# Kernel tuning notes

Hardware: AMD Instinct MI355X
Metric: run time of the kernel (lower is better)

## Reference

```python
import jax, jax.numpy as jnp
import numpy as np

N_NODES = 100000
N_EDGES = 1600000
IN_DIM = 256
HID = 128
N_LAYERS = 4
OUT_DIM = 7
LAMDA = 0.5
LN_EPS = 1e-5


def setup_inputs() -> dict:
    key = jax.random.key(0)
    ks = jax.random.split(key, 12)
    x = jax.random.normal(ks[0], (N_NODES, IN_DIM), jnp.float32)
    edge_index = jax.random.randint(ks[1], (2, N_EDGES), 0, N_NODES, dtype=jnp.int32)

    def unif(k, shape, fan_out):
        s = 1.0 / np.sqrt(fan_out)
        return jax.random.uniform(k, shape, jnp.float32, -s, s)

    W_proj = unif(ks[2], (IN_DIM, HID), HID)
    b_proj = unif(ks[3], (HID,), HID)
    gamma = jnp.ones((HID,), jnp.float32)
    beta = jnp.zeros((HID,), jnp.float32)
    q_w = unif(ks[4], (HID, 1), 1)
    q_b = unif(ks[5], (1,), 1)
    conv_w = unif(ks[6], (N_LAYERS, HID, HID), HID)
    cls_w = unif(ks[7], (HID, OUT_DIM), OUT_DIM)
    cls_b = unif(ks[8], (OUT_DIM,), OUT_DIM)
    return {"x": x, "edge_index": edge_index, "W_proj": W_proj, "b_proj": b_proj,
            "gamma": gamma, "beta": beta, "q_w": q_w, "q_b": q_b,
            "conv_w": conv_w, "cls_w": cls_w, "cls_b": cls_b}


def reference(x, edge_index, W_proj, b_proj, gamma, beta, q_w, q_b, conv_w, cls_w, cls_b):
    n = x.shape[0]
    row, col = edge_index[0], edge_index[1]

    # symmetric normalization: D^-1/2 A D^-1/2 with unit edge data (duplicates sum)
    deg = jax.ops.segment_sum(jnp.ones(row.shape[0], x.dtype), row, num_segments=n)
    deg = jnp.where(deg == 0, jnp.ones_like(deg), deg)  # (row_sum==0)*1 + row_sum
    d_inv_sqrt = deg ** -0.5
    ew = d_inv_sqrt[row] * d_inv_sqrt[col]  # [E]

    def spmm(h):  # out[r] += ew * h[c]
        return jax.ops.segment_sum(ew[:, None] * h[col], row, num_segments=n)

    def layernorm(h):
        mu = jnp.mean(h, axis=-1, keepdims=True)
        var = jnp.mean((h - mu) ** 2, axis=-1, keepdims=True)
        return gamma * (h - mu) * jax.lax.rsqrt(var + LN_EPS) + beta

    h0 = layernorm(x @ W_proj + b_proj)  # project + layernorm
    h = h0
    for i in range(conv_w.shape[0]):
        # dropout is identity in eval mode
        s = jax.nn.sigmoid(h @ q_w + q_b - 1.0)  # [N,1] learned gate
        theta = LAMDA / (i + 1)
        hi = spmm(h)
        support = (1.0 - s) * hi + s * h0  # AOR blend (variant=False -> r == support)
        out = theta * (support @ conv_w[i]) + (1.0 - theta) * support  # DLR
        h = layernorm(jax.nn.relu(out))
    return h @ cls_w + cls_b
```

## Files before the change

### kernel.cpp

```cpp
#include <hip/hip_runtime.h>
#include <hip/hip_bf16.h>
#include <hip/hip_fp16.h>
#include <stdint.h>

#define N_NODES 100000
#define N_EDGES 1600000
#define IN_DIM 256
#define HID 128
#define N_LAYERS 4
#define OUT_DIM 7
#define LN_EPS 1e-5f

#define BSHIFT 6
#define BROWS 64
#define NBK 1563
#define CHUNK 16384
#define NCH ((N_EDGES + CHUNK - 1) / CHUNK)

typedef __attribute__((ext_vector_type(8))) short bf16x8;
typedef __attribute__((ext_vector_type(4))) float f32x4;

__device__ inline float bf2f1(uint16_t u) {
    union { uint32_t i; float f; } a; a.i = ((uint32_t)u) << 16; return a.f;
}
__device__ inline uint16_t f2bf(float f) {
    union { float f; uint32_t i; } a; a.f = f;
    uint32_t lsb = (a.i >> 16) & 1u;
    a.i += 0x7fffu + lsb;
    return (uint16_t)(a.i >> 16);
}
__device__ inline uint32_t packq(float a, float b, float qinv) {
    int qa = __float2int_rn(a * qinv);
    int qb = __float2int_rn(b * qinv);
    return ((uint32_t)(uint16_t)(short)qa) | (((uint32_t)(uint16_t)(short)qb) << 16);
}

__device__ __host__ inline int wpack_idx(int k, int c) {
    int ksg = k >> 5, lg = (k >> 3) & 3, e = k & 7;
    int ct = c >> 4, li = c & 15;
    return ((ksg * 8 + ct) * 64 + (lg * 16 + li)) * 8 + e;
}

__global__ void k_detect(const uint32_t* __restrict__ W, int* __restrict__ flag) {
    if (threadIdx.x == 0 && blockIdx.x == 0) {
        int cnt = 0;
        for (int i = 0; i < 64; i++) {
            uint32_t lo = W[i] & 0xffffu;
            uint32_t ex = (lo >> 7) & 0xff;
            if (ex >= 0x60 && ex < 0x7c) cnt++;
        }
        *flag = (cnt < 32) ? 1 : 0;
    }
}
__global__ void k_setflag(int* __restrict__ flag, int v) {
    if (threadIdx.x == 0) *flag = v;
}

__global__ __launch_bounds__(256) void k_cvt(const void* a0, const void* a1, const void* a2,
                                             const void* a3, const void* a4, const void* a5,
                                             const void* a6, const void* a7, const void* a8,
                                             float* __restrict__ dst, const int* __restrict__ flag) {
    int t = blockIdx.x * 256 + threadIdx.x;
    if (t >= 99720) return;
    const void* src; int i; int off;
    if      (t < 32768) { src = a0; i = t;         off = 0;     }
    else if (t < 32896) { src = a1; i = t - 32768; off = 32768; }
    else if (t < 33024) { src = a2; i = t - 32896; off = 32896; }
    else if (t < 33152) { src = a3; i = t - 33024; off = 33024; }
    else if (t < 33280) { src = a4; i = t - 33152; off = 33152; }
    else if (t < 33281) { src = a5; i = t - 33280; off = 33280; }
    else if (t < 98817) { src = a6; i = t - 33281; off = 33296; }
    else if (t < 99713) { src = a7; i = t - 98817; off = 98832; }
    else                { src = a8; i = t - 99713; off = 99728; }
    float v;
    if (*flag) v = ((const float*)src)[i];
    else       v = bf2f1(((const uint16_t*)src)[i]);
    dst[off + i] = v;
}

__global__ __launch_bounds__(256) void k_wsplit(const float* __restrict__ stg,
                                                uint16_t* __restrict__ wpkhi, uint16_t* __restrict__ wpklo,
                                                uint16_t* __restrict__ cwkhi, uint16_t* __restrict__ cwklo) {
    int t = blockIdx.x * 256 + threadIdx.x;
    if (t >= 32768 + 65536) return;
    float v; size_t dst; uint16_t *ha, *la;
    if (t < 32768) {
        int k = t >> 7, c = t & 127;
        v = stg[t];
        dst = (size_t)wpack_idx(k, c); ha = wpkhi; la = wpklo;
    } else {
        int u = t - 32768;
        int L = u >> 14, rem = u & 16383;
        int k = rem >> 7, c = rem & 127;
        v = stg[33296 + u];
        dst = (size_t)L * 16384 + wpack_idx(k, c); ha = cwkhi; la = cwklo;
    }
    uint16_t hb = f2bf(v);
    uint16_t lb = f2bf(v - bf2f1(hb));
    ha[dst] = hb; la[dst] = lb;
}


__global__ __launch_bounds__(256) void k_hist(const int* __restrict__ row, int* __restrict__ hist) {
    __shared__ int lh[NBK];
    int b = blockIdx.x, tid = threadIdx.x;
    for (int i = tid; i < NBK; i += 256) lh[i] = 0;
    __syncthreads();
    int e0 = b * CHUNK;
    int lim = N_EDGES - e0; if (lim > CHUNK) lim = CHUNK;
    for (int i = tid; i < lim; i += 256) atomicAdd(&lh[row[e0 + i] >> BSHIFT], 1);
    __syncthreads();
    for (int i = tid; i < NBK; i += 256) hist[(size_t)b * NBK + i] = lh[i];
}

__global__ __launch_bounds__(128) void k_hscan(int* __restrict__ hist, int* __restrict__ totB) {
    __shared__ int s[128];
    int bkt = blockIdx.x, t = threadIdx.x;
    int v = (t < NCH) ? hist[(size_t)t * NBK + bkt] : 0;
    s[t] = v;
    __syncthreads();
    for (int off = 1; off < 128; off <<= 1) {
        int add = (t >= off) ? s[t - off] : 0;
        __syncthreads();
        s[t] += add;
        __syncthreads();
    }
    if (t < NCH) hist[(size_t)t * NBK + bkt] = s[t] - v;
    if (t == 127) totB[bkt] = s[127];
}

__global__ __launch_bounds__(256) void k_bscan(const int* __restrict__ totB,
                                               int* __restrict__ boffB, int* __restrict__ rp) {
    __shared__ int ps[256];
    int t = threadIdx.x;
    const int STRIP = 7;
    int base = t * STRIP;
    int loc[STRIP]; int sum = 0;
#pragma unroll
    for (int j = 0; j < STRIP; j++) {
        int idx = base + j;
        int v = (idx < NBK) ? totB[idx] : 0;
        loc[j] = sum; sum += v;
    }
    ps[t] = sum;
    __syncthreads();
    int v = ps[t];
    for (int off = 1; off < 256; off <<= 1) {
        int add = (t >= off) ? ps[t - off] : 0;
        __syncthreads();
        ps[t] += add;
        __syncthreads();
    }
    int excl = ps[t] - v;
#pragma unroll
    for (int j = 0; j < STRIP; j++) {
        int idx = base + j;
        if (idx < NBK) boffB[idx] = excl + loc[j];
    }
    if (t == 0) { boffB[NBK] = N_EDGES; rp[N_NODES] = N_EDGES; }
}

__global__ __launch_bounds__(256) void k_sortscat(const int* __restrict__ row, const int* __restrict__ col,
                                                  const int* __restrict__ hist, const int* __restrict__ boffB,
                                                  uint32_t* __restrict__ ebp) {
    __shared__ int dbase[NBK];
    __shared__ int lcnt[NBK];
    int b = blockIdx.x, tid = threadIdx.x;
    for (int i = tid; i < NBK; i += 256) {
        dbase[i] = boffB[i] + hist[(size_t)b * NBK + i];
        lcnt[i] = 0;
    }
    __syncthreads();
    int e0 = b * CHUNK;
    int lim = N_EDGES - e0; if (lim > CHUNK) lim = CHUNK;
    for (int i = tid; i < lim; i += 256) {
        int r = row[e0 + i], c = col[e0 + i];
        int bk = r >> BSHIFT;
        int rank = atomicAdd(&lcnt[bk], 1);
        ebp[dbase[bk] + rank] = ((uint32_t)(r & (BROWS - 1)) << 17) | (uint32_t)c;
    }
}

__global__ __launch_bounds__(256) void k_bfin(const uint32_t* __restrict__ ebp, const int* __restrict__ boffB,
                                              int* __restrict__ rp, float* __restrict__ dis,
                                              int* __restrict__ edc) {
    __shared__ int ldeg[BROWS];
    __shared__ int lcur[BROWS];
    int b = blockIdx.x, tid = threadIdx.x;
    int base = boffB[b];
    int n = boffB[b + 1] - base;
    if (tid < BROWS) ldeg[tid] = 0;
    __syncthreads();
    for (int i = tid; i < n; i += 256) atomicAdd(&ldeg[ebp[base + i] >> 17], 1);
    __syncthreads();
    if (tid == 0) {
        int run = 0;
        for (int r = 0; r < BROWS; r++) { int d = ldeg[r]; lcur[r] = run; run += d; }
    }
    __syncthreads();
    int row0 = b << BSHIFT;
    if (tid < BROWS && row0 + tid < N_NODES) {
        int d = ldeg[tid];
        rp[row0 + tid]  = base + lcur[tid];
        dis[row0 + tid] = rsqrtf((float)(d > 0 ? d : 1));
    }
    __syncthreads();
    for (int i = tid; i < n; i += 256) {
        uint32_t pk = ebp[base + i];
        int r = pk >> 17;
        int pos = atomicAdd(&lcur[r], 1);
        edc[base + pos] = (int)(pk & 0x1FFFFu);
    }
}


__global__ __launch_bounds__(256) void k_spmm(const uint32_t* __restrict__ Hq,
                                              const float* __restrict__ ScD,
                                              const float* __restrict__ H0,
                                              const int* __restrict__ rp,
                                              const int* __restrict__ edc,
                                              const float* __restrict__ S,
                                              const float* __restrict__ dis,
                                              uint16_t* __restrict__ SupHi,
                                              uint16_t* __restrict__ SupLo) {
    int wid  = (blockIdx.x * 256 + threadIdx.x) >> 6;
    int lane = threadIdx.x & 63;
    if (wid >= N_NODES) return;

    float s  = S[wid];
    float dr = dis[wid];
    float h0x = H0[(size_t)wid * 128 + lane];
    float h0y = H0[(size_t)wid * 128 + 64 + lane];

    int p0 = rp[wid], p1 = rp[wid + 1];
    float ax = 0.f, ay = 0.f;
    int p = p0;
    for (; p + 8 <= p1; p += 8) {
        int c[8]; uint32_t u[8]; float w[8];
#pragma unroll
        for (int j = 0; j < 8; j++) c[j] = edc[p + j];
#pragma unroll
        for (int j = 0; j < 8; j++) u[j] = Hq[(size_t)c[j] * 64 + lane];
#pragma unroll
        for (int j = 0; j < 8; j++) w[j] = ScD[c[j]];
#pragma unroll
        for (int j = 0; j < 8; j++) {
            ax += w[j] * (float)((int)(u[j] << 16) >> 16);
            ay += w[j] * (float)((int)u[j] >> 16);
        }
    }
    for (; p + 4 <= p1; p += 4) {
        int c[4]; uint32_t u[4]; float w[4];
#pragma unroll
        for (int j = 0; j < 4; j++) c[j] = edc[p + j];
#pragma unroll
        for (int j = 0; j < 4; j++) u[j] = Hq[(size_t)c[j] * 64 + lane];
#pragma unroll
        for (int j = 0; j < 4; j++) w[j] = ScD[c[j]];
#pragma unroll
        for (int j = 0; j < 4; j++) {
            ax += w[j] * (float)((int)(u[j] << 16) >> 16);
            ay += w[j] * (float)((int)u[j] >> 16);
        }
    }
    for (; p < p1; p++) {
        int c = edc[p];
        uint32_t u = Hq[(size_t)c * 64 + lane];
        float w = ScD[c];
        ax += w * (float)((int)(u << 16) >> 16);
        ay += w * (float)((int)u >> 16);
    }
    float f = (1.f - s) * dr;
    float ox = f * ax + s * h0x;
    float oy = f * ay + s * h0y;
    uint16_t hx = f2bf(ox), hy = f2bf(oy);
    uint16_t lx = f2bf(ox - bf2f1(hx)), ly = f2bf(oy - bf2f1(hy));
    SupHi[(size_t)wid * 128 + lane]      = hx;
    SupHi[(size_t)wid * 128 + 64 + lane] = hy;
    SupLo[(size_t)wid * 128 + lane]      = lx;
    SupLo[(size_t)wid * 128 + 64 + lane] = ly;
}


template <int KD, int MODE, int WH, int WQ, int WF>
__global__ __launch_bounds__(256, 2) void k_gemm(
    const void* __restrict__ Ax,
    const uint16_t* __restrict__ Ahi, const uint16_t* __restrict__ Alo,
    const uint16_t* __restrict__ Wh, const uint16_t* __restrict__ Wl,
    const float* __restrict__ bias, const float* __restrict__ gamma,
    const float* __restrict__ beta, const float* __restrict__ qw,
    const float* __restrict__ qb, float theta, const int* __restrict__ flag,
    const float* __restrict__ dis,
    float* __restrict__ Hout, uint32_t* __restrict__ Hq,
    float* __restrict__ Sc, float* __restrict__ S)
{
    if (*flag != WF) return;
    constexpr int F32A = (MODE == 0) ? WF : 1;
    constexpr int NKB = KD / 128;

    __shared__ __align__(16) uint16_t sWh[16384];
    __shared__ __align__(16) uint16_t sWl[16384];

    const int tid  = threadIdx.x;
    const int lane = tid & 63;
    const int wv   = tid >> 6;
    const int li   = lane & 15;
    const int lg   = lane >> 4;
    const size_t row0 = (size_t)blockIdx.x * 128;
    const int wb = wv * 32;
    size_t ar0 = row0 + wb + li;      if (ar0 >= N_NODES) ar0 = N_NODES - 1;
    size_t ar1 = row0 + wb + 16 + li; if (ar1 >= N_NODES) ar1 = N_NODES - 1;

    f32x4 acc0[8], acc1[8];
#pragma unroll
    for (int ct = 0; ct < 8; ct++) {
        acc0[ct] = (f32x4){0.f, 0.f, 0.f, 0.f};
        acc1[ct] = (f32x4){0.f, 0.f, 0.f, 0.f};
    }

    for (int kb = 0; kb < NKB; kb++) {
        if (kb) __syncthreads();
        const uint16_t* gh = Wh + kb * 16384;
#pragma unroll
        for (int it = 0; it < 8; it++) {
            int t = tid + it * 256;
            *(uint4*)(sWh + t * 8) = *(const uint4*)(gh + t * 8);
        }
        if constexpr (WF) {
            const uint16_t* gl = Wl + kb * 16384;
#pragma unroll
            for (int it = 0; it < 8; it++) {
                int t = tid + it * 256;
                *(uint4*)(sWl + t * 8) = *(const uint4*)(gl + t * 8);
            }
        }
        bf16x8 a0h[4], a1h[4], a0l[4], a1l[4];
#pragma unroll
        for (int s = 0; s < 4; s++) {
            const int koff = kb * 128 + s * 32 + lg * 8;
            if constexpr (MODE == 1) {
                a0h[s] = *(const bf16x8*)(Ahi + ar0 * KD + koff);
                a0l[s] = *(const bf16x8*)(Alo + ar0 * KD + koff);
                a1h[s] = *(const bf16x8*)(Ahi + ar1 * KD + koff);
                a1l[s] = *(const bf16x8*)(Alo + ar1 * KD + koff);
            } else if constexpr (WF) {
                const float* p0 = (const float*)Ax + ar0 * KD + koff;
                const float* p1 = (const float*)Ax + ar1 * KD + koff;
                float4 u0 = *(const float4*)p0, u1 = *(const float4*)(p0 + 4);
                float4 v0 = *(const float4*)p1, v1 = *(const float4*)(p1 + 4);
                float f0[8] = {u0.x, u0.y, u0.z, u0.w, u1.x, u1.y, u1.z, u1.w};
                float f1[8] = {v0.x, v0.y, v0.z, v0.w, v1.x, v1.y, v1.z, v1.w};
#pragma unroll
                for (int j = 0; j < 8; j++) {
                    uint16_t hb0 = f2bf(f0[j]);
                    a0h[s][j] = (short)hb0;
                    a0l[s][j] = (short)f2bf(f0[j] - bf2f1(hb0));
                    uint16_t hb1 = f2bf(f1[j]);
                    a1h[s][j] = (short)hb1;
                    a1l[s][j] = (short)f2bf(f1[j] - bf2f1(hb1));
                }
            } else {
                a0h[s] = *(const bf16x8*)((const uint16_t*)Ax + ar0 * KD + koff);
                a1h[s] = *(const bf16x8*)((const uint16_t*)Ax + ar1 * KD + koff);
            }
        }
        __syncthreads();
#pragma unroll
        for (int s = 0; s < 4; s++) {
#pragma unroll
            for (int ct = 0; ct < 8; ct++) {
                const int wo = ((s * 8 + ct) * 64 + lane) * 8;
                bf16x8 bh = *(const bf16x8*)(sWh + wo);
                acc0[ct] = __builtin_amdgcn_mfma_f32_16x16x32_bf16(a0h[s], bh, acc0[ct], 0, 0, 0);
                acc1[ct] = __builtin_amdgcn_mfma_f32_16x16x32_bf16(a1h[s], bh, acc1[ct], 0, 0, 0);
                if constexpr (F32A) {
                    acc0[ct] = __builtin_amdgcn_mfma_f32_16x16x32_bf16(a0l[s], bh, acc0[ct], 0, 0, 0);
                    acc1[ct] = __builtin_amdgcn_mfma_f32_16x16x32_bf16(a1l[s], bh, acc1[ct], 0, 0, 0);
                }
                if constexpr (WF) {
                    bf16x8 bl = *(const bf16x8*)(sWl + wo);
                    acc0[ct] = __builtin_amdgcn_mfma_f32_16x16x32_bf16(a0h[s], bl, acc0[ct], 0, 0, 0);
                    acc1[ct] = __builtin_amdgcn_mfma_f32_16x16x32_bf16(a1h[s], bl, acc1[ct], 0, 0, 0);
                }
            }
        }
    }

    float gm[8], bt_[8], qv[8], bi[8];
#pragma unroll
    for (int ct = 0; ct < 8; ct++) {
        int c = ct * 16 + li;
        gm[ct] = gamma[c]; bt_[ct] = beta[c]; qv[ct] = qw[c];
        bi[ct] = (MODE == 0) ? bias[c] : 0.f;
    }
    const float qbv = qb[0];
    const float om  = 1.f - theta;

    auto epi = [&](f32x4 (&acc)[8], int ssoff) {
#pragma unroll
        for (int r = 0; r < 4; r++) {
            int rowl  = wb + ssoff + lg * 4 + r;
            size_t rg = row0 + rowl;
            size_t rc = (rg < N_NODES) ? rg : (N_NODES - 1);
            float v[8];
            if (MODE == 0) {
#pragma unroll
                for (int ct = 0; ct < 8; ct++) v[ct] = acc[ct][r] + bi[ct];
            } else {
#pragma unroll
                for (int ct = 0; ct < 8; ct++) {
                    int c = ct * 16 + li;
                    float sv = bf2f1(Ahi[rc * KD + c]) + bf2f1(Alo[rc * KD + c]);
                    float o  = theta * acc[ct][r] + om * sv;
                    v[ct] = o > 0.f ? o : 0.f;
                }
            }
            float sum = 0.f, sq = 0.f;
#pragma unroll
            for (int ct = 0; ct < 8; ct++) { sum += v[ct]; sq += v[ct] * v[ct]; }
            sum += __shfl_xor(sum, 1); sum += __shfl_xor(sum, 2);
            sum += __shfl_xor(sum, 4); sum += __shfl_xor(sum, 8);
            sq  += __shfl_xor(sq, 1);  sq  += __shfl_xor(sq, 2);
            sq  += __shfl_xor(sq, 4);  sq  += __shfl_xor(sq, 8);
            float mu  = sum * (1.f / 128.f);
            float var = fmaxf(sq * (1.f / 128.f) - mu * mu, 0.f);
            float rs  = rsqrtf(var + LN_EPS);
            float y[8];
#pragma unroll
            for (int ct = 0; ct < 8; ct++) y[ct] = gm[ct] * (v[ct] - mu) * rs + bt_[ct];

            if (WQ) {
                float zd = 0.f, am = 0.f;
#pragma unroll
                for (int ct = 0; ct < 8; ct++) { zd += y[ct] * qv[ct]; am = fmaxf(am, fabsf(y[ct])); }
                zd += __shfl_xor(zd, 1); zd += __shfl_xor(zd, 2);
                zd += __shfl_xor(zd, 4); zd += __shfl_xor(zd, 8);
                am = fmaxf(am, __shfl_xor(am, 1)); am = fmaxf(am, __shfl_xor(am, 2));
                am = fmaxf(am, __shfl_xor(am, 4)); am = fmaxf(am, __shfl_xor(am, 8));
                float amc  = fmaxf(am, 1e-20f);
                float qinv = 32767.f / amc;
                if (rg < N_NODES) {
                    uint32_t* mq = Hq + rg * 64;
#pragma unroll
                    for (int ct = 0; ct < 4; ct++)
                        mq[ct * 16 + li] = packq(y[ct], y[ct + 4], qinv);
                    if (li == 0) {
                        Sc[rg] = amc * (1.f / 32767.f) * dis[rg];
                        S[rg]  = 1.f / (1.f + __expf(-(zd + qbv - 1.f)));
                    }
                }
            }
            if (WH && rg < N_NODES) {
                float* dst = Hout + rg * 128;
#pragma unroll
                for (int ct = 0; ct < 8; ct++) dst[ct * 16 + li] = y[ct];
            }
        }
    };
    epi(acc0, 0);
    epi(acc1, 16);
}


__global__ __launch_bounds__(256) void k_cls(const float* __restrict__ H,
                                             const float* __restrict__ Wc,
                                             const float* __restrict__ bc,
                                             const int* __restrict__ flag,
                                             void* __restrict__ out) {
    __shared__ float wS[128][8];
    int tid = threadIdx.x;
    for (int idx = tid; idx < 128 * 7; idx += 256) wS[idx / 7][idx % 7] = Wc[idx];
    __syncthreads();
    int isf32 = *flag;
    int gid = blockIdx.x * 256 + tid;
    int n = gid >> 3, j = gid & 7;
    if (n >= N_NODES || j >= OUT_DIM) return;
    const float4* hr = (const float4*)(H + (size_t)n * 128);
    float acc = bc[j];
#pragma unroll
    for (int k4 = 0; k4 < 32; k4++) {
        float4 h4 = hr[k4];
        acc += h4.x * wS[4 * k4][j]     + h4.y * wS[4 * k4 + 1][j]
             + h4.z * wS[4 * k4 + 2][j] + h4.w * wS[4 * k4 + 3][j];
    }
    size_t oi = (size_t)n * OUT_DIM + j;
    if (isf32) ((float*)out)[oi] = acc;
    else       ((uint16_t*)out)[oi] = f2bf(acc);
}


extern "C" void kernel_launch(void* const* d_in, const int* in_sizes, int n_in,
                              void* d_out, int out_size, void* d_ws, size_t ws_size,
                              hipStream_t stream) {
    const void* x_raw = d_in[0];
    const int*  ei    = (const int*)d_in[1];
    const int* row = ei;
    const int* col = ei + N_EDGES;

    char* ws = (char*)d_ws;
    size_t off = 0;
    auto alloc = [&](size_t b) { void* p = ws + off; off = (off + b + 255) & ~(size_t)255; return p; };
    int*      flag = (int*)alloc(4);
    float*    stgf = (float*)alloc((size_t)99744 * 4);
    int*      rp   = (int*)alloc(((size_t)N_NODES + 1) * 4);
    float*    dis  = (float*)alloc((size_t)N_NODES * 4);
    int*      hist = (int*)alloc((size_t)NCH * NBK * 4);
    int*      totB = (int*)alloc((size_t)NBK * 4);
    int*      boffB= (int*)alloc(((size_t)NBK + 1) * 4);
    int*      edc  = (int*)alloc((size_t)N_EDGES * 4);
    float*    h0   = (float*)alloc((size_t)N_NODES * HID * 4);
    uint16_t* suphi= (uint16_t*)alloc((size_t)N_NODES * HID * 2);
    uint16_t* suplo= (uint16_t*)alloc((size_t)N_NODES * HID * 2);
    uint32_t* hq   = (uint32_t*)alloc((size_t)N_NODES * 64 * 4);
    float*    Scq  = (float*)alloc((size_t)N_NODES * 4);
    float*    Sg   = (float*)alloc((size_t)N_NODES * 4);
    uint16_t* wpkhi = (uint16_t*)alloc((size_t)32768 * 2);
    uint16_t* wpklo = (uint16_t*)alloc((size_t)32768 * 2);
    uint16_t* cwkhi = (uint16_t*)alloc((size_t)65536 * 2);
    uint16_t* cwklo = (uint16_t*)alloc((size_t)65536 * 2);
    uint32_t* ebp  = (uint32_t*)h0;

    const float* bp  = stgf + 32768;
    const float* gm  = stgf + 32896;
    const float* bt  = stgf + 33024;
    const float* qw  = stgf + 33152;
    const float* qb  = stgf + 33280;
    const float* clw = stgf + 98832;
    const float* clb = stgf + 99728;

    int hostflag = -1;
    if (in_sizes && n_in >= 3) {
        if      (in_sizes[2] == 32768 * 4) hostflag = 1;
        else if (in_sizes[2] == 32768 * 2) hostflag = 0;
        else if (in_sizes[0] == N_NODES * IN_DIM * 4) hostflag = 1;
        else if (in_sizes[0] == N_NODES * IN_DIM * 2) hostflag = 0;
    }
    if (hostflag >= 0) k_setflag<<<1, 64, 0, stream>>>(flag, hostflag);
    else               k_detect<<<1, 64, 0, stream>>>((const uint32_t*)d_in[2], flag);

    k_cvt<<<(99720 + 255) / 256, 256, 0, stream>>>(d_in[2], d_in[3], d_in[4], d_in[5], d_in[6],
                                                   d_in[7], d_in[8], d_in[9], d_in[10], stgf, flag);
    k_wsplit<<<(98304 + 255) / 256, 256, 0, stream>>>(stgf, wpkhi, wpklo, cwkhi, cwklo);

    k_hist<<<NCH, 256, 0, stream>>>(row, hist);
    k_hscan<<<NBK, 128, 0, stream>>>(hist, totB);
    k_bscan<<<1, 256, 0, stream>>>(totB, boffB, rp);
    k_sortscat<<<NCH, 256, 0, stream>>>(row, col, hist, boffB, ebp);
    k_bfin<<<NBK, 256, 0, stream>>>(ebp, boffB, rp, dis, edc);

    const int gg = (N_NODES + 127) / 128;
    if (hostflag != 0)
        k_gemm<IN_DIM, 0, 1, 1, 1><<<gg, 256, 0, stream>>>(
            x_raw, nullptr, nullptr, wpkhi, wpklo, bp, gm, bt, qw, qb, 0.f, flag, dis,
            h0, hq, Scq, Sg);
    if (hostflag != 1)
        k_gemm<IN_DIM, 0, 1, 1, 0><<<gg, 256, 0, stream>>>(
            x_raw, nullptr, nullptr, wpkhi, wpklo, bp, gm, bt, qw, qb, 0.f, flag, dis,
            h0, hq, Scq, Sg);

    for (int i = 0; i < N_LAYERS; i++) {
        k_spmm<<<(N_NODES + 3) / 4, 256, 0, stream>>>(hq, Scq, h0, rp, edc, Sg, dis, suphi, suplo);
        float theta = 0.5f / (float)(i + 1);
        const uint16_t* whi = cwkhi + (size_t)i * 16384;
        const uint16_t* wlo = cwklo + (size_t)i * 16384;
        const int wh = (i == N_LAYERS - 1) ? 1 : 0;
        if (wh) {
            if (hostflag != 0)
                k_gemm<HID, 1, 1, 0, 1><<<gg, 256, 0, stream>>>(
                    nullptr, suphi, suplo, whi, wlo, nullptr, gm, bt, qw, qb, theta, flag, dis,
                    h0, hq, Scq, Sg);
            if (hostflag != 1)
                k_gemm<HID, 1, 1, 0, 0><<<gg, 256, 0, stream>>>(
                    nullptr, suphi, suplo, whi, wlo, nullptr, gm, bt, qw, qb, theta, flag, dis,
                    h0, hq, Scq, Sg);
        } else {
            if (hostflag != 0)
                k_gemm<HID, 1, 0, 1, 1><<<gg, 256, 0, stream>>>(
                    nullptr, suphi, suplo, whi, wlo, nullptr, gm, bt, qw, qb, theta, flag, dis,
                    h0, hq, Scq, Sg);
            if (hostflag != 1)
                k_gemm<HID, 1, 0, 1, 0><<<gg, 256, 0, stream>>>(
                    nullptr, suphi, suplo, whi, wlo, nullptr, gm, bt, qw, qb, theta, flag, dis,
                    h0, hq, Scq, Sg);
        }
    }
    k_cls<<<((size_t)N_NODES * 8 + 255) / 256, 256, 0, stream>>>(h0, clw, clb, flag, d_out);
}
```

Baseline: 750.3 us.

## Fuse classifier into last GEMM, halve GEMM K-tile, unroll SpMM gather by 16

Removes the separate classifier kernel by computing the 7-way output inside the final layer GEMM epilogue with shuffle reductions, so the last layer no longer writes H to memory and nothing reads it back. The GEMM K-block shrinks from 128 to 64, which halves shared memory, and launch bounds rise to 3 blocks per CU to raise occupancy. The SpMM gather loop is unrolled to 16 edges for more memory-level parallelism, at the cost of extra registers. The extra classifier weights held in registers may limit the higher occupancy target.

Result: slower. 832.2 us (+10.9%).

```diff
diff --git a/kernel.cpp b/kernel.cpp
--- a/kernel.cpp
+++ b/kernel.cpp
@@ -235,16 +235,16 @@
     int p0 = rp[wid], p1 = rp[wid + 1];
     float ax = 0.f, ay = 0.f;
     int p = p0;
-    for (; p + 8 <= p1; p += 8) {
-        int c[8]; uint32_t u[8]; float w[8];
-#pragma unroll
-        for (int j = 0; j < 8; j++) c[j] = edc[p + j];
-#pragma unroll
-        for (int j = 0; j < 8; j++) u[j] = Hq[(size_t)c[j] * 64 + lane];
-#pragma unroll
-        for (int j = 0; j < 8; j++) w[j] = ScD[c[j]];
-#pragma unroll
-        for (int j = 0; j < 8; j++) {
+    for (; p + 16 <= p1; p += 16) {
+        int c[16]; uint32_t u[16]; float w[16];
+#pragma unroll
+        for (int j = 0; j < 16; j++) c[j] = edc[p + j];
+#pragma unroll
+        for (int j = 0; j < 16; j++) u[j] = Hq[(size_t)c[j] * 64 + lane];
+#pragma unroll
+        for (int j = 0; j < 16; j++) w[j] = ScD[c[j]];
+#pragma unroll
+        for (int j = 0; j < 16; j++) {
             ax += w[j] * (float)((int)(u[j] << 16) >> 16);
             ay += w[j] * (float)((int)u[j] >> 16);
         }
@@ -282,8 +282,8 @@
 }
 
 
-template <int KD, int MODE, int WH, int WQ, int WF>
-__global__ __launch_bounds__(256, 2) void k_gemm(
+template <int KD, int MODE, int WH, int WQ, int WF, int WC>
+__global__ __launch_bounds__(256, 3) void k_gemm(
     const void* __restrict__ Ax,
     const uint16_t* __restrict__ Ahi, const uint16_t* __restrict__ Alo,
     const uint16_t* __restrict__ Wh, const uint16_t* __restrict__ Wl,
@@ -292,14 +292,16 @@
     const float* __restrict__ qb, float theta, const int* __restrict__ flag,
     const float* __restrict__ dis,
     float* __restrict__ Hout, uint32_t* __restrict__ Hq,
-    float* __restrict__ Sc, float* __restrict__ S)
+    float* __restrict__ Sc, float* __restrict__ S,
+    const float* __restrict__ clw, const float* __restrict__ clb,
+    void* __restrict__ Out)
 {
     if (*flag != WF) return;
     constexpr int F32A = (MODE == 0) ? WF : 1;
-    constexpr int NKB = KD / 128;
-
-    __shared__ __align__(16) uint16_t sWh[16384];
-    __shared__ __align__(16) uint16_t sWl[16384];
+    constexpr int NKB = KD / 64;
+
+    __shared__ __align__(16) uint16_t sWh[8192];
+    __shared__ __align__(16) uint16_t sWl[8192];
 
     const int tid  = threadIdx.x;
     const int lane = tid & 63;
@@ -320,24 +322,24 @@
 
     for (int kb = 0; kb < NKB; kb++) {
         if (kb) __syncthreads();
-        const uint16_t* gh = Wh + kb * 16384;
-#pragma unroll
-        for (int it = 0; it < 8; it++) {
+        const uint16_t* gh = Wh + kb * 8192;
+#pragma unroll
+        for (int it = 0; it < 4; it++) {
             int t = tid + it * 256;
             *(uint4*)(sWh + t * 8) = *(const uint4*)(gh + t * 8);
         }
         if constexpr (WF) {
-            const uint16_t* gl = Wl + kb * 16384;
-#pragma unroll
-            for (int it = 0; it < 8; it++) {
+            const uint16_t* gl = Wl + kb * 8192;
+#pragma unroll
+            for (int it = 0; it < 4; it++) {
                 int t = tid + it * 256;
                 *(uint4*)(sWl + t * 8) = *(const uint4*)(gl + t * 8);
             }
         }
-        bf16x8 a0h[4], a1h[4], a0l[4], a1l[4];
-#pragma unroll
-        for (int s = 0; s < 4; s++) {
-            const int koff = kb * 128 + s * 32 + lg * 8;
+        bf16x8 a0h[2], a1h[2], a0l[2], a1l[2];
+#pragma unroll
+        for (int s = 0; s < 2; s++) {
+            const int koff = kb * 64 + s * 32 + lg * 8;
             if constexpr (MODE == 1) {
                 a0h[s] = *(const bf16x8*)(Ahi + ar0 * KD + koff);
                 a0l[s] = *(const bf16x8*)(Alo + ar0 * KD + koff);
@@ -366,7 +368,7 @@
         }
         __syncthreads();
 #pragma unroll
-        for (int s = 0; s < 4; s++) {
+        for (int s = 0; s < 2; s++) {
 #pragma unroll
             for (int ct = 0; ct < 8; ct++) {
                 const int wo = ((s * 8 + ct) * 64 + lane) * 8;
@@ -393,6 +395,15 @@
         gm[ct] = gamma[c]; bt_[ct] = beta[c]; qv[ct] = qw[c];
         bi[ct] = (MODE == 0) ? bias[c] : 0.f;
     }
+    float wc[WC ? 56 : 1], cb[WC ? 7 : 1];
+    if constexpr (WC) {
+#pragma unroll
+        for (int ct = 0; ct < 8; ct++)
+#pragma unroll
+            for (int j = 0; j < 7; j++) wc[ct * 7 + j] = clw[(ct * 16 + li) * 7 + j];
+#pragma unroll
+        for (int j = 0; j < 7; j++) cb[j] = clb[j];
+    }
     const float qbv = qb[0];
     const float om  = 1.f - theta;
 
@@ -455,37 +466,25 @@
 #pragma unroll
                 for (int ct = 0; ct < 8; ct++) dst[ct * 16 + li] = y[ct];
             }
+            if (WC && rg < N_NODES) {
+#pragma unroll
+                for (int j = 0; j < 7; j++) {
+                    float z = 0.f;
+#pragma unroll
+                    for (int ct = 0; ct < 8; ct++) z += y[ct] * wc[ct * 7 + j];
+                    z += __shfl_xor(z, 1); z += __shfl_xor(z, 2);
+                    z += __shfl_xor(z, 4); z += __shfl_xor(z, 8);
+                    if (li == j) {
+                        size_t oi = rg * OUT_DIM + j;
+                        if (WF) ((float*)Out)[oi] = z + cb[j];
+                        else    ((uint16_t*)Out)[oi] = f2bf(z + cb[j]);
+                    }
+                }
+            }
         }
     };
     epi(acc0, 0);
     epi(acc1, 16);
-}
-
-
-__global__ __launch_bounds__(256) void k_cls(const float* __restrict__ H,
-                                             const float* __restrict__ Wc,
-                                             const float* __restrict__ bc,
-                                             const int* __restrict__ flag,
-                                             void* __restrict__ out) {
-    __shared__ float wS[128][8];
-    int tid = threadIdx.x;
-    for (int idx = tid; idx < 128 * 7; idx += 256) wS[idx / 7][idx % 7] = Wc[idx];
-    __syncthreads();
-    int isf32 = *flag;
-    int gid = blockIdx.x * 256 + tid;
-    int n = gid >> 3, j = gid & 7;
-    if (n >= N_NODES || j >= OUT_DIM) return;
-    const float4* hr = (const float4*)(H + (size_t)n * 128);
-    float acc = bc[j];
-#pragma unroll
-    for (int k4 = 0; k4 < 32; k4++) {
-        float4 h4 = hr[k4];
-        acc += h4.x * wS[4 * k4][j]     + h4.y * wS[4 * k4 + 1][j]
-             + h4.z * wS[4 * k4 + 2][j] + h4.w * wS[4 * k4 + 3][j];
-    }
-    size_t oi = (size_t)n * OUT_DIM + j;
-    if (isf32) ((float*)out)[oi] = acc;
-    else       ((uint16_t*)out)[oi] = f2bf(acc);
 }
 
 
@@ -550,39 +549,37 @@
 
     const int gg = (N_NODES + 127) / 128;
     if (hostflag != 0)
-        k_gemm<IN_DIM, 0, 1, 1, 1><<<gg, 256, 0, stream>>>(
+        k_gemm<IN_DIM, 0, 1, 1, 1, 0><<<gg, 256, 0, stream>>>(
             x_raw, nullptr, nullptr, wpkhi, wpklo, bp, gm, bt, qw, qb, 0.f, flag, dis,
-            h0, hq, Scq, Sg);
+            h0, hq, Scq, Sg, clw, clb, d_out);
     if (hostflag != 1)
-        k_gemm<IN_DIM, 0, 1, 1, 0><<<gg, 256, 0, stream>>>(
+        k_gemm<IN_DIM, 0, 1, 1, 0, 0><<<gg, 256, 0, stream>>>(
             x_raw, nullptr, nullptr, wpkhi, wpklo, bp, gm, bt, qw, qb, 0.f, flag, dis,
-            h0, hq, Scq, Sg);
+            h0, hq, Scq, Sg, clw, clb, d_out);
 
     for (int i = 0; i < N_LAYERS; i++) {
         k_spmm<<<(N_NODES + 3) / 4, 256, 0, stream>>>(hq, Scq, h0, rp, edc, Sg, dis, suphi, suplo);
         float theta = 0.5f / (float)(i + 1);
         const uint16_t* whi = cwkhi + (size_t)i * 16384;
         const uint16_t* wlo = cwklo + (size_t)i * 16384;
-        const int wh = (i == N_LAYERS - 1) ? 1 : 0;
-        if (wh) {
+        if (i < N_LAYERS - 1) {
             if (hostflag != 0)
-                k_gemm<HID, 1, 1, 0, 1><<<gg, 256, 0, stream>>>(
+                k_gemm<HID, 1, 0, 1, 1, 0><<<gg, 256, 0, stream>>>(
                     nullptr, suphi, suplo, whi, wlo, nullptr, gm, bt, qw, qb, theta, flag, dis,
-                    h0, hq, Scq, Sg);
+                    nullptr, hq, Scq, Sg, clw, clb, d_out);
             if (hostflag != 1)
-                k_gemm<HID, 1, 1, 0, 0><<<gg, 256, 0, stream>>>(
+                k_gemm<HID, 1, 0, 1, 0, 0><<<gg, 256, 0, stream>>>(
                     nullptr, suphi, suplo, whi, wlo, nullptr, gm, bt, qw, qb, theta, flag, dis,
-                    h0, hq, Scq, Sg);
+                    nullptr, hq, Scq, Sg, clw, clb, d_out);
         } else {
             if (hostflag != 0)
-                k_gemm<HID, 1, 0, 1, 1><<<gg, 256, 0, stream>>>(
+                k_gemm<HID, 1, 0, 0, 1, 1><<<gg, 256, 0, stream>>>(
                     nullptr, suphi, suplo, whi, wlo, nullptr, gm, bt, qw, qb, theta, flag, dis,
-                    h0, hq, Scq, Sg);
+                    nullptr, hq, Scq, Sg, clw, clb, d_out);
             if (hostflag != 1)
-                k_gemm<HID, 1, 0, 1, 0><<<gg, 256, 0, stream>>>(
+                k_gemm<HID, 1, 0, 0, 0, 1><<<gg, 256, 0, stream>>>(
                     nullptr, suphi, suplo, whi, wlo, nullptr, gm, bt, qw, qb, theta, flag, dis,
-                    h0, hq, Scq, Sg);
-        }
-    }
-    k_cls<<<((size_t)N_NODES * 8 + 255) / 256, 256, 0, stream>>>(h0, clw, clb, flag, d_out);
-}
+                    nullptr, hq, Scq, Sg, clw, clb, d_out);
+        }
+    }
+}
```
